# Kernel optimization log

Measured on AMD Instinct MI355X. Metric: run time of the kernel, lower is better.

## Reference

```python
import jax, jax.numpy as jnp
import numpy as np

T = 8           # timesteps
VTH = 1.0       # IFNode v_threshold (spikingjelly default)
ALPHA = 2.0     # ATan surrogate alpha (spikingjelly default)
BN_EPS = 1e-5

@jax.custom_vjp
def atan_spike(x):
    # Heaviside(x) with ATan surrogate gradient
    return (x >= 0.0).astype(x.dtype)

def _spike_fwd(x):
    return atan_spike(x), x

def _spike_bwd(x, g):
    sg = (ALPHA / 2.0) / (1.0 + (jnp.pi / 2.0 * ALPHA * x) ** 2)
    return (g * sg,)

atan_spike.defvjp(_spike_fwd, _spike_bwd)

def maxpool2x2(x):  # [B,C,H,W] -> [B,C,H/2,W/2]
    return jax.lax.reduce_window(x, -jnp.inf, jax.lax.max,
                                 (1, 1, 2, 2), (1, 1, 2, 2), 'VALID')

def setup_inputs() -> dict:
    key = jax.random.key(0)
    k0, k1, k2 = jax.random.split(key, 3)
    B, C = 128, 128
    x = jax.random.uniform(k0, (B, 1, 28, 28), jnp.float32)
    conv_w = jax.random.normal(k1, (C, 1, 3, 3), jnp.float32) * 0.3
    bn_gamma = jnp.ones((C,), jnp.float32)
    bn_beta = jnp.zeros((C,), jnp.float32)
    bn_mean = jnp.zeros((C,), jnp.float32)
    bn_var = jnp.ones((C,), jnp.float32)
    fc_w = jax.random.normal(k2, (10, C * 14 * 14), jnp.float32) * 0.01
    return dict(x=x, conv_w=conv_w, bn_gamma=bn_gamma, bn_beta=bn_beta,
                bn_mean=bn_mean, bn_var=bn_var, fc_w=fc_w)

def reference(x, conv_w, bn_gamma, bn_beta, bn_mean, bn_var, fc_w):
    B = x.shape[0]
    # stateless conv + BN(eval): identical for all T repeated timesteps, compute once
    y = jax.lax.conv_general_dilated(
        x, conv_w, window_strides=(1, 1), padding=((1, 1), (1, 1)),
        dimension_numbers=('NCHW', 'OIHW', 'NCHW'))
    scale = (bn_gamma * jax.lax.rsqrt(bn_var + BN_EPS))[None, :, None, None]
    pre = (y - bn_mean[None, :, None, None]) * scale + bn_beta[None, :, None, None]

    def step(carry, _):
        v1, v2 = carry
        # IFNode 1: integrate, fire, hard reset to 0
        v1 = v1 + pre
        s1 = atan_spike(v1 - VTH)
        v1 = v1 * (1.0 - s1)
        f = maxpool2x2(s1).reshape(B, -1)        # [B, C*14*14]
        # IFNode 2 after linear
        v2 = v2 + f @ fc_w.T                      # [B, 10]
        s2 = atan_spike(v2 - VTH)
        v2 = v2 * (1.0 - s2)
        return (v1, v2), s2

    v1_0 = jnp.zeros_like(pre)
    v2_0 = jnp.zeros((B, 10), pre.dtype)
    _, spikes = jax.lax.scan(step, (v1_0, v2_0), None, length=T)  # [T,B,10]
    return spikes.mean(0)  # firing rate [B,10]
```

## Files before the change

kernel.cpp:

```cpp
#include <hip/hip_runtime.h>

#define T 8
#define VTH 1.0f
#define BN_EPS 1e-5f
#define CG 8
#define NG (128 / CG)

__global__ __launch_bounds__(256) void k_conv_if_pool(
    const float* __restrict__ x,
    const float* __restrict__ conv_w,
    const float* __restrict__ gamma,
    const float* __restrict__ beta,
    const float* __restrict__ mean,
    const float* __restrict__ var,
    unsigned char* __restrict__ f)
{
    __shared__ float xs[30 * 30];
    const int blk = blockIdx.x;
    const int b = blk / NG;
    const int g = blk - b * NG;
    const int tid = threadIdx.x;

    for (int i = tid; i < 900; i += 256) xs[i] = 0.0f;
    __syncthreads();
    const float* xb = x + b * 784;
    for (int i = tid; i < 784; i += 256) {
        int h = i / 28, w = i - h * 28;
        xs[(h + 1) * 30 + (w + 1)] = xb[i];
    }
    __syncthreads();

    if (tid >= 196) return;
    const int ph = tid / 14, pw = tid - ph * 14;

    float patch[16];
    const int base = (2 * ph) * 30 + 2 * pw;
    #pragma unroll
    for (int r = 0; r < 4; r++)
        #pragma unroll
        for (int cc = 0; cc < 4; cc++)
            patch[r * 4 + cc] = xs[base + r * 30 + cc];

    #pragma unroll
    for (int ci = 0; ci < CG; ci++) {
        const int c = g * CG + ci;
        const float* wc = conv_w + c * 9;
        float wv[9];
        #pragma unroll
        for (int i = 0; i < 9; i++) wv[i] = wc[i];
        const float sc = gamma[c] * rsqrtf(var[c] + BN_EPS);
        const float sh = beta[c] - mean[c] * sc;

        unsigned int bits = 0;
        #pragma unroll
        for (int dy = 0; dy < 2; dy++) {
            #pragma unroll
            for (int dx = 0; dx < 2; dx++) {
                float y = 0.0f;
                #pragma unroll
                for (int kh = 0; kh < 3; kh++)
                    #pragma unroll
                    for (int kw = 0; kw < 3; kw++)
                        y += patch[(dy + kh) * 4 + (dx + kw)] * wv[kh * 3 + kw];
                const float p = y * sc + sh;
                float v = 0.0f;
                #pragma unroll
                for (int t = 0; t < T; t++) {
                    v += p;
                    if (v - VTH >= 0.0f) { bits |= (1u << t); v = 0.0f; }
                }
            }
        }
        f[(b * 128 + c) * 196 + tid] = (unsigned char)bits;
    }
}

__global__ __launch_bounds__(512) void k_fc_if(
    const unsigned char* __restrict__ f,
    const float* __restrict__ fc_w,
    float* __restrict__ out)
{
    const int blk = blockIdx.x;
    const int b = blk >> 1;
    const int og = blk & 1;
    const int tid = threadIdx.x;
    const int lane = tid & 63;
    const int wave = tid >> 6;

    const unsigned int* fm = (const unsigned int*)(f + b * 25088);
    const float4* fw0 = (const float4*)(fc_w + (og * 5 + 0) * 25088);
    const float4* fw1 = (const float4*)(fc_w + (og * 5 + 1) * 25088);
    const float4* fw2 = (const float4*)(fc_w + (og * 5 + 2) * 25088);
    const float4* fw3 = (const float4*)(fc_w + (og * 5 + 3) * 25088);
    const float4* fw4 = (const float4*)(fc_w + (og * 5 + 4) * 25088);

    float acc[T][5];
    #pragma unroll
    for (int t = 0; t < T; t++)
        #pragma unroll
        for (int o = 0; o < 5; o++) acc[t][o] = 0.0f;

    for (int i = tid; i < 25088 / 4; i += 512) {
        const unsigned int m4 = fm[i];
        float4 w[5] = {fw0[i], fw1[i], fw2[i], fw3[i], fw4[i]};
        #pragma unroll
        for (int j = 0; j < 4; j++) {
            const float wj[5] = {((const float*)&w[0])[j], ((const float*)&w[1])[j],
                                 ((const float*)&w[2])[j], ((const float*)&w[3])[j],
                                 ((const float*)&w[4])[j]};
            #pragma unroll
            for (int t = 0; t < T; t++) {
                const float bit = (float)((m4 >> (8 * j + t)) & 1u);
                #pragma unroll
                for (int o = 0; o < 5; o++)
                    acc[t][o] = fmaf(bit, wj[o], acc[t][o]);
            }
        }
    }

    __shared__ float red[8][T * 5];
    #pragma unroll
    for (int t = 0; t < T; t++)
        #pragma unroll
        for (int o = 0; o < 5; o++) {
            float v = acc[t][o];
            #pragma unroll
            for (int off = 32; off > 0; off >>= 1)
                v += __shfl_down(v, off, 64);
            if (lane == 0) red[wave][t * 5 + o] = v;
        }
    __syncthreads();

    __shared__ float tot[T * 5];
    if (tid < T * 5) {
        float s = 0.0f;
        #pragma unroll
        for (int wv = 0; wv < 8; wv++) s += red[wv][tid];
        tot[tid] = s;
    }
    __syncthreads();

    if (tid < 5) {
        float v2 = 0.0f, cnt = 0.0f;
        #pragma unroll
        for (int t = 0; t < T; t++) {
            v2 += tot[t * 5 + tid];
            if (v2 - VTH >= 0.0f) { cnt += 1.0f; v2 = 0.0f; }
        }
        out[b * 10 + og * 5 + tid] = cnt * (1.0f / (float)T);
    }
}

extern "C" void kernel_launch(void* const* d_in, const int* in_sizes, int n_in,
                              void* d_out, int out_size, void* d_ws, size_t ws_size,
                              hipStream_t stream) {
    const float* x      = (const float*)d_in[0];
    const float* conv_w = (const float*)d_in[1];
    const float* gamma  = (const float*)d_in[2];
    const float* beta   = (const float*)d_in[3];
    const float* mean   = (const float*)d_in[4];
    const float* var    = (const float*)d_in[5];
    const float* fc_w   = (const float*)d_in[6];
    float* out = (float*)d_out;

    unsigned char* f = (unsigned char*)d_ws;

    k_conv_if_pool<<<128 * NG, 256, 0, stream>>>(x, conv_w, gamma, beta, mean, var, f);
    k_fc_if<<<128 * 2, 512, 0, stream>>>(f, fc_w, out);
}
```

Baseline: 117.2 us.

## Pack two images per conv block, use LUT for IF spikes, widen FC blocks

The conv/IF/pool kernel now handles two images per block with 448 threads, so fewer threads sit idle (392 of 448 active instead of 196 of 256). It replaces the per-timestep branchy integrate-and-fire loop with a count of sub-threshold steps that indexes a 64-bit lookup table of spike patterns, exploiting constant input per step. The FC kernel doubles its block size to 1024 threads with a 16-wave reduction. The LUT shortcut assumes the spike pattern depends only on that count, and the larger blocks may raise register pressure and lower occupancy.

Result: faster. 110.3 us (-5.9%).

```diff
diff --git a/kernel.cpp b/kernel.cpp
--- a/kernel.cpp
+++ b/kernel.cpp
@@ -6,7 +6,9 @@
 #define CG 8
 #define NG (128 / CG)
 
-__global__ __launch_bounds__(256) void k_conv_if_pool(
+#define IF_LUT 0x804020108824AAFFull
+
+__global__ __launch_bounds__(448) void k_conv_if_pool(
     const float* __restrict__ x,
     const float* __restrict__ conv_w,
     const float* __restrict__ gamma,
@@ -15,31 +17,40 @@
     const float* __restrict__ var,
     unsigned char* __restrict__ f)
 {
-    __shared__ float xs[30 * 30];
+    __shared__ float xs[2][30 * 30];
     const int blk = blockIdx.x;
-    const int b = blk / NG;
-    const int g = blk - b * NG;
+    const int bp = blk / NG;
+    const int g = blk - bp * NG;
     const int tid = threadIdx.x;
 
-    for (int i = tid; i < 900; i += 256) xs[i] = 0.0f;
+    for (int i = tid; i < 900; i += 448) { xs[0][i] = 0.0f; xs[1][i] = 0.0f; }
     __syncthreads();
-    const float* xb = x + b * 784;
-    for (int i = tid; i < 784; i += 256) {
-        int h = i / 28, w = i - h * 28;
-        xs[(h + 1) * 30 + (w + 1)] = xb[i];
+    const float* xb = x + bp * 1568;
+    for (int i = tid; i < 1568; i += 448) {
+        const int bl = (i >= 784) ? 1 : 0;
+        const int j = i - bl * 784;
+        const int h = j / 28, w = j - h * 28;
+        xs[bl][(h + 1) * 30 + (w + 1)] = xb[i];
     }
     __syncthreads();
 
-    if (tid >= 196) return;
-    const int ph = tid / 14, pw = tid - ph * 14;
+    if (tid >= 392) return;
+    const int bl = (tid >= 196) ? 1 : 0;
+    const int pos = tid - bl * 196;
+    const int ph = pos / 14, pw = pos - ph * 14;
+    const int b = bp * 2 + bl;
 
     float patch[16];
-    const int base = (2 * ph) * 30 + 2 * pw;
-    #pragma unroll
-    for (int r = 0; r < 4; r++)
+    {
+        const float* xr = &xs[bl][(2 * ph) * 30 + 2 * pw];
         #pragma unroll
-        for (int cc = 0; cc < 4; cc++)
-            patch[r * 4 + cc] = xs[base + r * 30 + cc];
+        for (int r = 0; r < 4; r++)
+            #pragma unroll
+            for (int cc = 0; cc < 4; cc++)
+                patch[r * 4 + cc] = xr[r * 30 + cc];
+    }
+
+    unsigned char* frow = f + (b * 128 + g * CG) * 196 + pos;
 
     #pragma unroll
     for (int ci = 0; ci < CG; ci++) {
@@ -51,9 +62,9 @@
         const float sc = gamma[c] * rsqrtf(var[c] + BN_EPS);
         const float sh = beta[c] - mean[c] * sc;
 
-        unsigned int bits = 0;
+        float p[4];
         #pragma unroll
-        for (int dy = 0; dy < 2; dy++) {
+        for (int dy = 0; dy < 2; dy++)
             #pragma unroll
             for (int dx = 0; dx < 2; dx++) {
                 float y = 0.0f;
@@ -62,20 +73,28 @@
                     #pragma unroll
                     for (int kw = 0; kw < 3; kw++)
                         y += patch[(dy + kh) * 4 + (dx + kw)] * wv[kh * 3 + kw];
-                const float p = y * sc + sh;
-                float v = 0.0f;
-                #pragma unroll
-                for (int t = 0; t < T; t++) {
-                    v += p;
-                    if (v - VTH >= 0.0f) { bits |= (1u << t); v = 0.0f; }
-                }
+                p[dy * 2 + dx] = y * sc + sh;
             }
+
+        unsigned int bits = 0;
+        #pragma unroll
+        for (int cell = 0; cell < 4; cell++) {
+            float s = 0.0f;
+            int cnt = 0;
+            #pragma unroll
+            for (int t = 0; t < T; t++) {
+                s += p[cell];
+                cnt += (s < VTH) ? 1 : 0;
+            }
+            const unsigned int bm = (cnt >= 8) ? 0u
+                : (unsigned int)((IF_LUT >> ((cnt & 7) * 8)) & 0xFFull);
+            bits |= bm;
         }
-        f[(b * 128 + c) * 196 + tid] = (unsigned char)bits;
+        frow[ci * 196] = (unsigned char)bits;
     }
 }
 
-__global__ __launch_bounds__(512) void k_fc_if(
+__global__ __launch_bounds__(1024) void k_fc_if(
     const unsigned char* __restrict__ f,
     const float* __restrict__ fc_w,
     float* __restrict__ out)
@@ -100,7 +119,7 @@
         #pragma unroll
         for (int o = 0; o < 5; o++) acc[t][o] = 0.0f;
 
-    for (int i = tid; i < 25088 / 4; i += 512) {
+    for (int i = tid; i < 25088 / 4; i += 1024) {
         const unsigned int m4 = fm[i];
         float4 w[5] = {fw0[i], fw1[i], fw2[i], fw3[i], fw4[i]};
         #pragma unroll
@@ -118,7 +137,7 @@
         }
     }
 
-    __shared__ float red[8][T * 5];
+    __shared__ float red[16][T * 5];
     #pragma unroll
     for (int t = 0; t < T; t++)
         #pragma unroll
@@ -135,7 +154,7 @@
     if (tid < T * 5) {
         float s = 0.0f;
         #pragma unroll
-        for (int wv = 0; wv < 8; wv++) s += red[wv][tid];
+        for (int wv = 0; wv < 16; wv++) s += red[wv][tid];
         tot[tid] = s;
     }
     __syncthreads();
@@ -165,6 +184,6 @@
 
     unsigned char* f = (unsigned char*)d_ws;
 
-    k_conv_if_pool<<<128 * NG, 256, 0, stream>>>(x, conv_w, gamma, beta, mean, var, f);
-    k_fc_if<<<128 * 2, 512, 0, stream>>>(f, fc_w, out);
+    k_conv_if_pool<<<64 * NG, 448, 0, stream>>>(x, conv_w, gamma, beta, mean, var, f);
+    k_fc_if<<<128 * 2, 1024, 0, stream>>>(f, fc_w, out);
 }
```
